# Kernel tuning notes

Hardware: AMD Instinct MI355X
Metric: run time of the kernel (lower is better)

The kernel has to match this reference:

```python
import jax, jax.numpy as jnp
import numpy as np
import math

MUL = 64
E = 65536
IRREPS1 = [(MUL, 0), (MUL, 1), (MUL, 2)]  # parities e,o,e (parity only selects paths)
IRREPS2 = [(1, 0), (1, 1), (1, 2)]
# (i_in1, i_in2, l_out) for each 'uvu' instruction, in e3nn enumeration order
INSTR = [(0,0,0),(0,1,1),(0,2,2),(1,0,1),(1,1,0),(1,1,1),(1,1,2),(1,2,1),(1,2,2),
         (2,0,2),(2,1,1),(2,1,2),(2,2,0),(2,2,1),(2,2,2)]

def _cg(l1, l2, l3, m1, m2, m3):
    # Condon-Shortley Clebsch-Gordan <l1 m1 l2 m2 | l3 m3> (Racah formula)
    if m1 + m2 != m3:
        return 0.0
    f = math.factorial
    pre = ((2*l3+1) * f(l3+l1-l2) * f(l3-l1+l2) * f(l1+l2-l3) / f(l1+l2+l3+1)) ** 0.5
    pre *= (f(l3+m3)*f(l3-m3)*f(l1-m1)*f(l1+m1)*f(l2-m2)*f(l2+m2)) ** 0.5
    kmin = max(0, l2-l3-m1, l1-l3+m2)
    kmax = min(l1+l2-l3, l1-m1, l2+m2)
    s = sum((-1)**k / (f(k)*f(l1+l2-l3-k)*f(l1-m1-k)*f(l2+m2-k)*f(l3-l2+m1+k)*f(l3-l1-m2+k))
            for k in range(kmin, kmax+1))
    return pre * s

def _w3j_complex(l1, l2, l3):
    w = np.zeros((2*l1+1, 2*l2+1, 2*l3+1))
    for m1 in range(-l1, l1+1):
        for m2 in range(-l2, l2+1):
            m3 = -(m1+m2)
            if abs(m3) <= l3:
                w[m1+l1, m2+l2, m3+l3] = ((-1)**(l1-l2-m3)) * _cg(l1,l2,l3,m1,m2,m1+m2) / (2*l3+1)**0.5
    return w

def _Q(l):
    # complex -> real spherical-harmonic change of basis (rows/cols ordered m=-l..l)
    q = np.zeros((2*l+1, 2*l+1), dtype=complex)
    q[l, l] = 1.0
    s2 = math.sqrt(2.0)
    for m in range(1, l+1):
        q[l+m, l+m] = (-1)**m / s2
        q[l+m, l-m] = 1.0 / s2
        q[l-m, l-m] = 1j / s2
        q[l-m, l+m] = -1j * (-1)**m / s2
    return q

def _real_w3j(l1, l2, l3):
    T = np.einsum('aA,bB,cC,ABC->abc', _Q(l1), _Q(l2), _Q(l3), _w3j_complex(l1,l2,l3).astype(complex))
    re, im = T.real, T.imag
    T = re if np.linalg.norm(re) >= np.linalg.norm(im) else im  # invariant tensor is real up to a phase
    return (T / np.linalg.norm(T)).astype(np.float32)  # unit Frobenius norm, as e3nn's wigner_3j

CG_TABLES = [_real_w3j(IRREPS1[i][1], IRREPS2[j][1], lo) for (i, j, lo) in INSTR]
# irrep_normalization='component' -> alpha = 2*lo+1; path_normalization='element' -> fan-in = mul_in2 = 1
PATH_W = [math.sqrt(2*lo+1) for (_, _, lo) in INSTR]
OFF1 = [0, MUL, MUL*4]          # offsets of 0e/1o/2e blocks in x1 (dims 64,192,320)
OFF2 = [0, 1, 4]                # offsets of 0e/1o/2e blocks in x2
DIM1, DIM2 = MUL*9, 9
WDIM = MUL*len(INSTR)           # 960 per-edge weights
ODIM = MUL*sum(2*lo+1 for (_,_,lo) in INSTR)  # 3264


def setup_inputs() -> dict:
    key = jax.random.key(0)
    k1, k2, k3 = jax.random.split(key, 3)
    return {
        'x1': jax.random.normal(k1, (E, DIM1), dtype=jnp.float32),
        'x2': jax.random.normal(k2, (E, DIM2), dtype=jnp.float32),
        'weight': jax.random.normal(k3, (E, WDIM), dtype=jnp.float32),
    }


def reference(x1, x2, weight):
    n = x1.shape[0]
    outs = []
    for idx, (i, j, lo) in enumerate(INSTR):
        l1, l2 = IRREPS1[i][1], IRREPS2[j][1]
        u = x1[:, OFF1[i]:OFF1[i] + MUL*(2*l1+1)].reshape(n, MUL, 2*l1+1)  # [z,u,i]
        v = x2[:, OFF2[j]:OFF2[j] + (2*l2+1)]                              # [z,j] (mul2=1)
        w = weight[:, idx*MUL:(idx+1)*MUL]                                  # [z,u] per-edge 'uvu' weights
        C = jnp.asarray(CG_TABLES[idx] * PATH_W[idx])
        t = jnp.einsum('ijk,zui,zj->zuk', C, u, v)
        outs.append((t * w[:, :, None]).reshape(n, MUL*(2*lo+1)))
    return jnp.concatenate(outs, axis=1)
```

## Files before the change

### kernel.cpp

```cpp
#include <hip/hip_runtime.h>
#include <hip/hip_bf16.h>


struct Tbl { double v[5][5][5]; };
struct CMat { double re[5][5]; double im[5][5]; };

constexpr double cfact(int n) {
    double r = 1.0;
    for (int i = 2; i <= n; ++i) r *= (double)i;
    return r;
}

constexpr double csqrt(double x) {
    if (x <= 0.0) return 0.0;
    double g = x > 1.0 ? x : 1.0;
    for (int i = 0; i < 100; ++i) g = 0.5 * (g + x / g);
    return g;
}

constexpr int cparity(int k) { return (((k % 2) + 2) % 2 == 0) ? 1 : -1; }

constexpr double ccg(int l1, int l2, int l3, int m1, int m2, int m3) {
    if (m1 + m2 != m3) return 0.0;
    double pre = csqrt((2.0 * l3 + 1.0) * cfact(l3 + l1 - l2) * cfact(l3 - l1 + l2) *
                       cfact(l1 + l2 - l3) / cfact(l1 + l2 + l3 + 1));
    pre *= csqrt(cfact(l3 + m3) * cfact(l3 - m3) * cfact(l1 - m1) * cfact(l1 + m1) *
                 cfact(l2 - m2) * cfact(l2 + m2));
    int kmin = 0;
    if (l2 - l3 - m1 > kmin) kmin = l2 - l3 - m1;
    if (l1 - l3 + m2 > kmin) kmin = l1 - l3 + m2;
    int kmax = l1 + l2 - l3;
    if (l1 - m1 < kmax) kmax = l1 - m1;
    if (l2 + m2 < kmax) kmax = l2 + m2;
    double s = 0.0;
    for (int k = kmin; k <= kmax; ++k) {
        s += (double)cparity(k) /
             (cfact(k) * cfact(l1 + l2 - l3 - k) * cfact(l1 - m1 - k) * cfact(l2 + m2 - k) *
              cfact(l3 - l2 + m1 + k) * cfact(l3 - l1 - m2 + k));
    }
    return pre * s;
}

constexpr Tbl cw3j_complex(int l1, int l2, int l3) {
    Tbl w{};
    for (int m1 = -l1; m1 <= l1; ++m1)
        for (int m2 = -l2; m2 <= l2; ++m2) {
            int m3 = -(m1 + m2);
            if (m3 >= -l3 && m3 <= l3) {
                w.v[m1 + l1][m2 + l2][m3 + l3] =
                    (double)cparity(l1 - l2 - m3) * ccg(l1, l2, l3, m1, m2, m1 + m2) /
                    csqrt(2.0 * l3 + 1.0);
            }
        }
    return w;
}

constexpr CMat cQ(int l) {
    CMat q{};
    q.re[l][l] = 1.0;
    double s2 = csqrt(2.0);
    for (int m = 1; m <= l; ++m) {
        q.re[l + m][l + m] = (double)cparity(m) / s2;
        q.re[l + m][l - m] = 1.0 / s2;
        q.im[l - m][l - m] = 1.0 / s2;
        q.im[l - m][l + m] = -(double)cparity(m) / s2;
    }
    return q;
}

constexpr Tbl creal_w3j(int l1, int l2, int l3) {
    const CMat q1 = cQ(l1), q2 = cQ(l2), q3 = cQ(l3);
    const Tbl w = cw3j_complex(l1, l2, l3);
    const int n1 = 2 * l1 + 1, n2 = 2 * l2 + 1, n3 = 2 * l3 + 1;
    Tbl t1re{}, t1im{};
    for (int A = 0; A < n1; ++A)
        for (int B = 0; B < n2; ++B)
            for (int c = 0; c < n3; ++c) {
                double re = 0.0, im = 0.0;
                for (int C = 0; C < n3; ++C) {
                    re += w.v[A][B][C] * q3.re[c][C];
                    im += w.v[A][B][C] * q3.im[c][C];
                }
                t1re.v[A][B][c] = re;
                t1im.v[A][B][c] = im;
            }
    Tbl t2re{}, t2im{};
    for (int A = 0; A < n1; ++A)
        for (int b = 0; b < n2; ++b)
            for (int c = 0; c < n3; ++c) {
                double re = 0.0, im = 0.0;
                for (int B = 0; B < n2; ++B) {
                    re += q2.re[b][B] * t1re.v[A][B][c] - q2.im[b][B] * t1im.v[A][B][c];
                    im += q2.re[b][B] * t1im.v[A][B][c] + q2.im[b][B] * t1re.v[A][B][c];
                }
                t2re.v[A][b][c] = re;
                t2im.v[A][b][c] = im;
            }
    Tbl Tre{}, Tim{};
    for (int a = 0; a < n1; ++a)
        for (int b = 0; b < n2; ++b)
            for (int c = 0; c < n3; ++c) {
                double re = 0.0, im = 0.0;
                for (int A = 0; A < n1; ++A) {
                    re += q1.re[a][A] * t2re.v[A][b][c] - q1.im[a][A] * t2im.v[A][b][c];
                    im += q1.re[a][A] * t2im.v[A][b][c] + q1.im[a][A] * t2re.v[A][b][c];
                }
                Tre.v[a][b][c] = re;
                Tim.v[a][b][c] = im;
            }
    double nre = 0.0, nim = 0.0;
    for (int a = 0; a < n1; ++a)
        for (int b = 0; b < n2; ++b)
            for (int c = 0; c < n3; ++c) {
                nre += Tre.v[a][b][c] * Tre.v[a][b][c];
                nim += Tim.v[a][b][c] * Tim.v[a][b][c];
            }
    const bool useRe = (nre >= nim);
    const double norm = csqrt(useRe ? nre : nim);
    const double scale = csqrt(2.0 * l3 + 1.0) / norm;
    Tbl out{};
    for (int a = 0; a < n1; ++a)
        for (int b = 0; b < n2; ++b)
            for (int c = 0; c < n3; ++c) {
                float t32 = (float)((useRe ? Tre.v[a][b][c] : Tim.v[a][b][c]) / norm);
                out.v[a][b][c] = (double)t32 * csqrt(2.0 * l3 + 1.0);
                (void)scale;
            }
    return out;
}

constexpr Tbl CG[15] = {
    creal_w3j(0, 0, 0), creal_w3j(0, 1, 1), creal_w3j(0, 2, 2), creal_w3j(1, 0, 1),
    creal_w3j(1, 1, 0), creal_w3j(1, 1, 1), creal_w3j(1, 1, 2), creal_w3j(1, 2, 1),
    creal_w3j(1, 2, 2), creal_w3j(2, 0, 2), creal_w3j(2, 1, 1), creal_w3j(2, 1, 2),
    creal_w3j(2, 2, 0), creal_w3j(2, 2, 1), creal_w3j(2, 2, 2)};


#define MUL_C 64
#define DIM1_C 576
#define DIM2_C 9
#define WDIM_C 960
#define ODIM_C 3264

template <int IDX, int N1, int N2, int N3>
__device__ __forceinline__ void do_path(const float (&a)[N1], const float (&b)[N2], float w,
                                        float* __restrict__ op) {
    float t[N3];
#pragma unroll
    for (int k = 0; k < N3; ++k) t[k] = 0.0f;
#pragma unroll
    for (int i = 0; i < N1; ++i) {
#pragma unroll
        for (int j = 0; j < N2; ++j) {
            const float p = a[i] * b[j];
#pragma unroll
            for (int k = 0; k < N3; ++k) {
                constexpr const Tbl& T = CG[IDX];
                const float c = (float)T.v[i][j][k];
                if (c != 0.0f) t[k] = fmaf(c, p, t[k]);
            }
        }
    }
#pragma unroll
    for (int k = 0; k < N3; ++k) op[k] = t[k] * w;
}

__global__ __launch_bounds__(256) void tp_kernel(const float* __restrict__ x1,
                                                 const float* __restrict__ x2,
                                                 const float* __restrict__ wgt,
                                                 float* __restrict__ out, int n) {
    const int tid = blockIdx.x * blockDim.x + threadIdx.x;
    const int e = tid >> 6;
    const int u = tid & 63;
    if (e >= n) return;

    const float* __restrict__ x1e = x1 + (size_t)e * DIM1_C;
    const float* __restrict__ x2e = x2 + (size_t)e * DIM2_C;
    const float* __restrict__ we = wgt + (size_t)e * WDIM_C;
    float* __restrict__ oe = out + (size_t)e * ODIM_C;

    float a0[1], a1[3], a2[5];
    a0[0] = x1e[u];
#pragma unroll
    for (int i = 0; i < 3; ++i) a1[i] = x1e[64 + u * 3 + i];
#pragma unroll
    for (int i = 0; i < 5; ++i) a2[i] = x1e[256 + u * 5 + i];

    float b0[1], b1[3], b2[5];
    b0[0] = x2e[0];
#pragma unroll
    for (int j = 0; j < 3; ++j) b1[j] = x2e[1 + j];
#pragma unroll
    for (int j = 0; j < 5; ++j) b2[j] = x2e[4 + j];

    do_path<0, 1, 1, 1>(a0, b0, we[0 * 64 + u], oe + 0 + u * 1);
    do_path<1, 1, 3, 3>(a0, b1, we[1 * 64 + u], oe + 64 + u * 3);
    do_path<2, 1, 5, 5>(a0, b2, we[2 * 64 + u], oe + 256 + u * 5);
    do_path<3, 3, 1, 3>(a1, b0, we[3 * 64 + u], oe + 576 + u * 3);
    do_path<4, 3, 3, 1>(a1, b1, we[4 * 64 + u], oe + 768 + u * 1);
    do_path<5, 3, 3, 3>(a1, b1, we[5 * 64 + u], oe + 832 + u * 3);
    do_path<6, 3, 3, 5>(a1, b1, we[6 * 64 + u], oe + 1024 + u * 5);
    do_path<7, 3, 5, 3>(a1, b2, we[7 * 64 + u], oe + 1344 + u * 3);
    do_path<8, 3, 5, 5>(a1, b2, we[8 * 64 + u], oe + 1536 + u * 5);
    do_path<9, 5, 1, 5>(a2, b0, we[9 * 64 + u], oe + 1856 + u * 5);
    do_path<10, 5, 3, 3>(a2, b1, we[10 * 64 + u], oe + 2176 + u * 3);
    do_path<11, 5, 3, 5>(a2, b1, we[11 * 64 + u], oe + 2368 + u * 5);
    do_path<12, 5, 5, 1>(a2, b2, we[12 * 64 + u], oe + 2688 + u * 1);
    do_path<13, 5, 5, 3>(a2, b2, we[13 * 64 + u], oe + 2752 + u * 3);
    do_path<14, 5, 5, 5>(a2, b2, we[14 * 64 + u], oe + 2944 + u * 5);
}

extern "C" void kernel_launch(void* const* d_in, const int* in_sizes, int n_in, void* d_out,
                              int out_size, void* d_ws, size_t ws_size, hipStream_t stream) {
    const float* x1 = (const float*)d_in[0];
    const float* x2 = (const float*)d_in[1];
    const float* w = (const float*)d_in[2];
    float* out = (float*)d_out;
    const int n = in_sizes[0] / DIM1_C;
    const int threads = n * 64;
    const int block = 256;
    const int grid = (threads + block - 1) / block;
    tp_kernel<<<grid, block, 0, stream>>>(x1, x2, w, out, n);
}
```

Baseline: 247.3 us.

## Stage outputs in LDS and stream coalesced float4 stores with persistent prefetching

```diff
diff --git a/kernel.cpp b/kernel.cpp
--- a/kernel.cpp
+++ b/kernel.cpp
@@ -117,14 +117,12 @@
             }
     const bool useRe = (nre >= nim);
     const double norm = csqrt(useRe ? nre : nim);
-    const double scale = csqrt(2.0 * l3 + 1.0) / norm;
     Tbl out{};
     for (int a = 0; a < n1; ++a)
         for (int b = 0; b < n2; ++b)
             for (int c = 0; c < n3; ++c) {
                 float t32 = (float)((useRe ? Tre.v[a][b][c] : Tim.v[a][b][c]) / norm);
                 out.v[a][b][c] = (double)t32 * csqrt(2.0 * l3 + 1.0);
-                (void)scale;
             }
     return out;
 }
@@ -136,15 +134,46 @@
     creal_w3j(2, 2, 0), creal_w3j(2, 2, 1), creal_w3j(2, 2, 2)};
 
 
-#define MUL_C 64
 #define DIM1_C 576
 #define DIM2_C 9
 #define WDIM_C 960
 #define ODIM_C 3264
 
+__device__ __forceinline__ void lds_fence() {
+    __builtin_amdgcn_sched_barrier(0);
+    asm volatile("s_waitcnt lgkmcnt(0)" ::: "memory");
+    __builtin_amdgcn_sched_barrier(0);
+}
+
+struct Frag {
+    float a0[1], a1[3], a2[5];
+    float b0[1], b1[3], b2[5];
+    float w[15];
+};
+
+__device__ __forceinline__ void load_frag(const float* __restrict__ x1,
+                                          const float* __restrict__ x2,
+                                          const float* __restrict__ wgt, int e, int u, Frag& f) {
+    const float* __restrict__ x1e = x1 + (size_t)e * DIM1_C;
+    const float* __restrict__ x2e = x2 + (size_t)e * DIM2_C;
+    const float* __restrict__ we = wgt + (size_t)e * WDIM_C;
+    f.a0[0] = x1e[u];
+#pragma unroll
+    for (int i = 0; i < 3; ++i) f.a1[i] = x1e[64 + u * 3 + i];
+#pragma unroll
+    for (int i = 0; i < 5; ++i) f.a2[i] = x1e[256 + u * 5 + i];
+    f.b0[0] = x2e[0];
+#pragma unroll
+    for (int j = 0; j < 3; ++j) f.b1[j] = x2e[1 + j];
+#pragma unroll
+    for (int j = 0; j < 5; ++j) f.b2[j] = x2e[4 + j];
+#pragma unroll
+    for (int p = 0; p < 15; ++p) f.w[p] = we[p * 64 + u];
+}
+
 template <int IDX, int N1, int N2, int N3>
 __device__ __forceinline__ void do_path(const float (&a)[N1], const float (&b)[N2], float w,
-                                        float* __restrict__ op) {
+                                        float* op) {
     float t[N3];
 #pragma unroll
     for (int k = 0; k < N3; ++k) t[k] = 0.0f;
@@ -165,49 +194,66 @@
     for (int k = 0; k < N3; ++k) op[k] = t[k] * w;
 }
 
-__global__ __launch_bounds__(256) void tp_kernel(const float* __restrict__ x1,
-                                                 const float* __restrict__ x2,
-                                                 const float* __restrict__ wgt,
-                                                 float* __restrict__ out, int n) {
-    const int tid = blockIdx.x * blockDim.x + threadIdx.x;
-    const int e = tid >> 6;
-    const int u = tid & 63;
+__device__ __forceinline__ void compute_to_lds(const Frag& f, float* buf, int u) {
+    do_path<0, 1, 1, 1>(f.a0, f.b0, f.w[0], buf + 0 + u * 1);
+    do_path<1, 1, 3, 3>(f.a0, f.b1, f.w[1], buf + 64 + u * 3);
+    do_path<2, 1, 5, 5>(f.a0, f.b2, f.w[2], buf + 256 + u * 5);
+    do_path<3, 3, 1, 3>(f.a1, f.b0, f.w[3], buf + 576 + u * 3);
+    do_path<4, 3, 3, 1>(f.a1, f.b1, f.w[4], buf + 768 + u * 1);
+    do_path<5, 3, 3, 3>(f.a1, f.b1, f.w[5], buf + 832 + u * 3);
+    do_path<6, 3, 3, 5>(f.a1, f.b1, f.w[6], buf + 1024 + u * 5);
+    do_path<7, 3, 5, 3>(f.a1, f.b2, f.w[7], buf + 1344 + u * 3);
+    do_path<8, 3, 5, 5>(f.a1, f.b2, f.w[8], buf + 1536 + u * 5);
+    do_path<9, 5, 1, 5>(f.a2, f.b0, f.w[9], buf + 1856 + u * 5);
+    do_path<10, 5, 3, 3>(f.a2, f.b1, f.w[10], buf + 2176 + u * 3);
+    do_path<11, 5, 3, 5>(f.a2, f.b1, f.w[11], buf + 2368 + u * 5);
+    do_path<12, 5, 5, 1>(f.a2, f.b2, f.w[12], buf + 2688 + u * 1);
+    do_path<13, 5, 5, 3>(f.a2, f.b2, f.w[13], buf + 2752 + u * 3);
+    do_path<14, 5, 5, 5>(f.a2, f.b2, f.w[14], buf + 2944 + u * 5);
+}
+
+__device__ __forceinline__ void stream_out(const float* buf, float* __restrict__ out, int e,
+                                           int u) {
+    float4* __restrict__ outv = (float4*)(out + (size_t)e * ODIM_C);
+    const float4* sv = (const float4*)buf;
+#pragma unroll
+    for (int it = 0; it < 12; ++it) outv[u + it * 64] = sv[u + it * 64];
+    if (u < 48) outv[u + 768] = sv[u + 768];
+}
+
+__global__ __launch_bounds__(64) void tp_kernel(const float* __restrict__ x1,
+                                                const float* __restrict__ x2,
+                                                const float* __restrict__ wgt,
+                                                float* __restrict__ out, int n) {
+    __shared__ __align__(16) float bufA[ODIM_C];
+    __shared__ __align__(16) float bufB[ODIM_C];
+    const int u = threadIdx.x & 63;
+    const int stride = gridDim.x;
+    int e = (int)blockIdx.x;
     if (e >= n) return;
 
-    const float* __restrict__ x1e = x1 + (size_t)e * DIM1_C;
-    const float* __restrict__ x2e = x2 + (size_t)e * DIM2_C;
-    const float* __restrict__ we = wgt + (size_t)e * WDIM_C;
-    float* __restrict__ oe = out + (size_t)e * ODIM_C;
-
-    float a0[1], a1[3], a2[5];
-    a0[0] = x1e[u];
-#pragma unroll
-    for (int i = 0; i < 3; ++i) a1[i] = x1e[64 + u * 3 + i];
-#pragma unroll
-    for (int i = 0; i < 5; ++i) a2[i] = x1e[256 + u * 5 + i];
-
-    float b0[1], b1[3], b2[5];
-    b0[0] = x2e[0];
-#pragma unroll
-    for (int j = 0; j < 3; ++j) b1[j] = x2e[1 + j];
-#pragma unroll
-    for (int j = 0; j < 5; ++j) b2[j] = x2e[4 + j];
-
-    do_path<0, 1, 1, 1>(a0, b0, we[0 * 64 + u], oe + 0 + u * 1);
-    do_path<1, 1, 3, 3>(a0, b1, we[1 * 64 + u], oe + 64 + u * 3);
-    do_path<2, 1, 5, 5>(a0, b2, we[2 * 64 + u], oe + 256 + u * 5);
-    do_path<3, 3, 1, 3>(a1, b0, we[3 * 64 + u], oe + 576 + u * 3);
-    do_path<4, 3, 3, 1>(a1, b1, we[4 * 64 + u], oe + 768 + u * 1);
-    do_path<5, 3, 3, 3>(a1, b1, we[5 * 64 + u], oe + 832 + u * 3);
-    do_path<6, 3, 3, 5>(a1, b1, we[6 * 64 + u], oe + 1024 + u * 5);
-    do_path<7, 3, 5, 3>(a1, b2, we[7 * 64 + u], oe + 1344 + u * 3);
-    do_path<8, 3, 5, 5>(a1, b2, we[8 * 64 + u], oe + 1536 + u * 5);
-    do_path<9, 5, 1, 5>(a2, b0, we[9 * 64 + u], oe + 1856 + u * 5);
-    do_path<10, 5, 3, 3>(a2, b1, we[10 * 64 + u], oe + 2176 + u * 3);
-    do_path<11, 5, 3, 5>(a2, b1, we[11 * 64 + u], oe + 2368 + u * 5);
-    do_path<12, 5, 5, 1>(a2, b2, we[12 * 64 + u], oe + 2688 + u * 1);
-    do_path<13, 5, 5, 3>(a2, b2, we[13 * 64 + u], oe + 2752 + u * 3);
-    do_path<14, 5, 5, 5>(a2, b2, we[14 * 64 + u], oe + 2944 + u * 5);
+    Frag f, g;
+    load_frag(x1, x2, wgt, e, u, f);
+
+    while (true) {
+        compute_to_lds(f, bufA, u);
+        int en = e + stride;
+        bool more = en < n;
+        if (more) load_frag(x1, x2, wgt, en, u, g);
+        lds_fence();
+        stream_out(bufA, out, e, u);
+        if (!more) return;
+        e = en;
+
+        compute_to_lds(g, bufB, u);
+        en = e + stride;
+        more = en < n;
+        if (more) load_frag(x1, x2, wgt, en, u, f);
+        lds_fence();
+        stream_out(bufB, out, e, u);
+        if (!more) return;
+        e = en;
+    }
 }
 
 extern "C" void kernel_launch(void* const* d_in, const int* in_sizes, int n_in, void* d_out,
@@ -217,8 +263,7 @@
     const float* w = (const float*)d_in[2];
     float* out = (float*)d_out;
     const int n = in_sizes[0] / DIM1_C;
-    const int threads = n * 64;
-    const int block = 256;
-    const int grid = (threads + block - 1) / block;
-    tp_kernel<<<grid, block, 0, stream>>>(x1, x2, w, out, n);
-}
+    int grid = 6 * 256;
+    if (grid > n) grid = n;
+    tp_kernel<<<grid, 64, 0, stream>>>(x1, x2, w, out, n);
+}
```

Measured after the change: 252.4 us. +2.1%, slower.
